# Kernel tuning notes

Hardware: AMD Instinct MI355X
Metric: run time of the kernel (lower is better)

## Reference

```python
import jax, jax.numpy as jnp
import numpy as np

N = 100000   # nodes
E = 600000   # edges (no self loops by construction)
F = 64       # feature_size
H = 2 * F    # hidden_size = 128
G = 32       # graphs in batch
L = N // G   # nodes per graph (equal-size graphs)
NEG_SLOPE = 0.2  # GATConv default leaky_relu slope


def setup_inputs() -> dict:
    key = jax.random.key(0)
    ks = jax.random.split(key, 16)
    x = jax.random.normal(ks[0], (N, F), jnp.float32)
    # edges guaranteed to have no self loops (PyG GAT removes then re-adds them)
    src = jax.random.randint(ks[1], (E,), 0, N)
    off = jax.random.randint(ks[2], (E,), 1, N)
    dst = (src + off) % N
    edge_index = jnp.stack([src, dst]).astype(jnp.int32)
    batch = (jnp.arange(N) // L).astype(jnp.int32)
    sF = 1.0 / np.sqrt(F)
    sH = 1.0 / np.sqrt(H)
    return {
        "x": x, "edge_index": edge_index, "batch": batch,
        "W0": jax.random.normal(ks[3], (F, H), jnp.float32) * sF,
        "b0": jnp.zeros((H,), jnp.float32),
        "Wg": jax.random.normal(ks[4], (H, H), jnp.float32) * sH,
        "att_src": jax.random.normal(ks[5], (H,), jnp.float32) * sH,
        "att_dst": jax.random.normal(ks[6], (H,), jnp.float32) * sH,
        "W1": jax.random.normal(ks[7], (H, H), jnp.float32) * sH,
        "b1": jnp.zeros((H,), jnp.float32),
        "W2": jax.random.normal(ks[8], (H, H), jnp.float32) * sH,
        "b2": jnp.zeros((H,), jnp.float32),
        "Wr": jax.random.normal(ks[9], (H, F), jnp.float32) * sH,
        "br": jnp.zeros((F,), jnp.float32),
    }


def _gcn(x, row, col, w, W, b):
    # PyG GCNConv (normalize=True); edges already include self loops, w holds edge weights.
    xw = x @ W
    deg = jax.ops.segment_sum(w, col, num_segments=N)
    dinv = jnp.where(deg > 0, deg, 1.0) ** -0.5
    dinv = jnp.where(deg > 0, dinv, 0.0)
    norm = dinv[row] * w * dinv[col]                      # [E+N]
    out = jax.ops.segment_sum(xw[row] * norm[:, None], col, num_segments=N)
    return out + b


def reference(x, edge_index, batch, W0, b0, Wg, att_src, att_dst, W1, b1, W2, b2, Wr, br):
    row, col = edge_index[0], edge_index[1]
    loops = jnp.arange(N, dtype=edge_index.dtype)
    row_f = jnp.concatenate([row, loops])                 # [E+N] with self loops
    col_f = jnp.concatenate([col, loops])

    # initial GCNConv (gcn_norm adds self loops with weight 1) + relu
    x = jax.nn.relu(_gcn(x, row_f, col_f, jnp.ones(E + N, x.dtype), W0, b0))

    # GATConv attention (heads=1); node output is discarded in the torch module
    xg = x @ Wg
    a_s = xg @ att_src
    a_d = xg @ att_dst
    e = jax.nn.leaky_relu(a_s[row_f] + a_d[col_f], NEG_SLOPE)
    m = jax.ops.segment_max(e, col_f, num_segments=N)
    ex = jnp.exp(e - m[col_f])
    alpha = ex / jax.ops.segment_sum(ex, col_f, num_segments=N)[col_f]

    # gcn_norm's add_remaining_self_loops replaces self-loop weights with 1.0
    w = alpha.at[E:].set(1.0)

    x = jax.nn.relu(_gcn(x, row_f, col_f, w, W1, b1))
    x = jax.nn.relu(_gcn(x, row_f, col_f, w, W2, b2))

    # readout: Dropout (eval -> identity) + Linear
    out = x @ Wr + br                                     # [N, F]

    # unbatch + pad_sequence (batch_first=True); batch ids are sorted
    counts = jax.ops.segment_sum(jnp.ones(N, jnp.int32), batch, num_segments=G)
    starts = jnp.concatenate([jnp.zeros(1, jnp.int32), jnp.cumsum(counts)[:-1].astype(jnp.int32)])
    pos = jnp.arange(N, dtype=jnp.int32) - starts[batch]
    emb = jnp.zeros((G, L, F), out.dtype).at[batch, pos].set(out)
    return emb
```

## Files before the change

kernel.cpp:

```cpp
#include <hip/hip_runtime.h>
#include <hip/hip_bf16.h>
#include <hip/hip_fp16.h>
#include <math.h>

#define NN 100000
#define EE 600000
#define FF 64
#define HH 128
#define CHUNK 1024
#define NCHUNK ((NN + CHUNK - 1) / CHUNK)
#define NCHUNKS_M (NN / 16)
#define PREP_ITEMS (NN * FF / 4 + 49280)

typedef unsigned short u16;
typedef unsigned int u32;
typedef __attribute__((ext_vector_type(8))) short bf16x8;
typedef __attribute__((ext_vector_type(4))) float f32x4;

__device__ __forceinline__ u16 f2bf(float f) {
    __hip_bfloat16 h = __float2bfloat16(f);
    return *(u16*)&h;
}
__device__ __forceinline__ float bf2f(u16 u) {
    unsigned int t = ((unsigned int)u) << 16;
    return *(float*)&t;
}
__device__ __forceinline__ u32 enc_meta(int r, float w) {
    u16 hb = __half_as_ushort(__float2half(w));
    return ((u32)r << 15) | (hb & 0x7fffu);
}
__device__ __forceinline__ void dec_meta(u32 u, int& r, float& w) {
    r = (int)(u >> 15);
    w = __half2float(__ushort_as_half((u16)(u & 0x7fffu)));
}


__global__ void build_k(const int* __restrict__ col, int* __restrict__ cnt,
                        const float* __restrict__ W0, const float* __restrict__ W1,
                        const float* __restrict__ W2, const float* __restrict__ Wr,
                        const float* __restrict__ Wg, const float* __restrict__ att_src,
                        const float* __restrict__ att_dst, const float* __restrict__ x,
                        u16* __restrict__ Wt0, u16* __restrict__ Wt1,
                        u16* __restrict__ Wt2, u16* __restrict__ Wtr,
                        float* __restrict__ vs, float* __restrict__ vd,
                        u16* __restrict__ xb) {
    int i = blockIdx.x * 256 + threadIdx.x;
    if (i < EE) {
        atomicAdd(&cnt[col[i]], 1);
        return;
    }
    i -= EE;
    if (i < NN * FF / 4) {
        float4 v = ((const float4*)x)[i];
        ushort4 o;
        o.x = f2bf(v.x); o.y = f2bf(v.y); o.z = f2bf(v.z); o.w = f2bf(v.w);
        ((ushort4*)xb)[i] = o;
        return;
    }
    i -= NN * FF / 4;
    if (i < 8192) {
        int n = i >> 6, k = i & 63;
        Wt0[i] = f2bf(W0[k * 128 + n]);
        return;
    }
    i -= 8192;
    if (i < 16384) {
        int n = i >> 7, k = i & 127;
        Wt1[i] = f2bf(W1[k * 128 + n]);
        return;
    }
    i -= 16384;
    if (i < 16384) {
        int n = i >> 7, k = i & 127;
        Wt2[i] = f2bf(W2[k * 128 + n]);
        return;
    }
    i -= 16384;
    if (i < 8192) {
        int n = i >> 7, k = i & 127;
        Wtr[i] = f2bf(Wr[k * 64 + n]);
        return;
    }
    i -= 8192;
    if (i < HH) {
        float s1 = 0.f, s2 = 0.f;
        for (int j = 0; j < HH; j++) {
            float w = Wg[i * HH + j];
            s1 += w * att_src[j];
            s2 += w * att_dst[j];
        }
        vs[i] = s1;
        vd[i] = s2;
    }
}

__global__ void chunksum_k(const int* __restrict__ cnt, int* __restrict__ chunk_sum,
                           float* __restrict__ dinv1) {
    int b = blockIdx.x, t = threadIdx.x;
    int base = b * CHUNK + t * 4;
    int s = 0;
    #pragma unroll
    for (int i = 0; i < 4; i++) {
        int idx = base + i;
        if (idx < NN) {
            int cv = cnt[idx];
            s += cv;
            dinv1[idx] = rsqrtf((float)cv + 1.0f);
        }
    }
    __shared__ int sm[4];
    for (int d = 32; d > 0; d >>= 1) s += __shfl_down(s, d);
    if ((t & 63) == 0) sm[t >> 6] = s;
    __syncthreads();
    if (t == 0) chunk_sum[b] = sm[0] + sm[1] + sm[2] + sm[3];
}

__global__ void colptr_k(const int* __restrict__ cnt, const int* __restrict__ chunk_sum,
                         int* __restrict__ col_ptr, int* __restrict__ cursor) {
    int b = blockIdx.x, t = threadIdx.x;
    __shared__ int base_off;
    if (t == 0) {
        int run = 0;
        for (int i = 0; i < b; i++) run += chunk_sum[i];
        base_off = run;
        if (b == 0) col_ptr[NN] = EE;
    }
    int base = b * CHUNK + t * 4;
    int c[4]; int tot = 0;
    #pragma unroll
    for (int i = 0; i < 4; i++) { int idx = base + i; c[i] = (idx < NN) ? cnt[idx] : 0; tot += c[i]; }
    __shared__ int s[256];
    s[t] = tot;
    __syncthreads();
    for (int d = 1; d < 256; d <<= 1) {
        int v = (t >= d) ? s[t - d] : 0;
        __syncthreads();
        s[t] += v;
        __syncthreads();
    }
    int excl = s[t] - tot;
    int off = base_off + excl;
    int pre = 0;
    #pragma unroll
    for (int i = 0; i < 4; i++) {
        int idx = base + i;
        if (idx < NN) {
            col_ptr[idx] = off + pre;
            cursor[idx] = off + pre;
        }
        pre += c[i];
    }
}

__global__ void fill_k(const int* __restrict__ row, const int* __restrict__ col,
                       int* __restrict__ cursor, const float* __restrict__ dinv1,
                       u32* __restrict__ meta1) {
    int e = blockIdx.x * 256 + threadIdx.x;
    if (e < EE) {
        int r = row[e], c = col[e];
        int slot = atomicAdd(&cursor[c], 1);
        meta1[slot] = enc_meta(r, dinv1[r] * dinv1[c]);
    }
}


__global__ __launch_bounds__(256, 8) void aggx_k(
    const u16* __restrict__ xb, const int* __restrict__ col_ptr, const u32* __restrict__ meta1,
    const float* __restrict__ dinv1, u16* __restrict__ xout) {
    int wid = threadIdx.x >> 6, lane = threadIdx.x & 63;
    int sub = lane >> 5;
    int c = blockIdx.x * 8 + wid * 2 + sub;
    int hl = lane & 31;
    int g = hl >> 3;
    int ch = (hl & 7) << 3;
    int beg = col_ptr[c], end = col_ptr[c + 1];
    float acc[8] = {};

    int pA = beg + g, pB = pA + 4;
    int rA = 0, rB = 0; float wA = 0.f, wB = 0.f;
    if (pA < end) dec_meta(meta1[pA], rA, wA);
    if (pB < end) dec_meta(meta1[pB], rB, wB);
    while (pA < end) {
        bool hb = pB < end;
        bf16x8 vA = *(const bf16x8*)&xb[(size_t)rA * FF + ch];
        bf16x8 vB;
        if (hb) vB = *(const bf16x8*)&xb[(size_t)rB * FF + ch];
        int pA2 = pA + 8, pB2 = pB + 8;
        int rA2 = 0, rB2 = 0; float wA2 = 0.f, wB2 = 0.f;
        if (pA2 < end) dec_meta(meta1[pA2], rA2, wA2);
        if (pB2 < end) dec_meta(meta1[pB2], rB2, wB2);
        #pragma unroll
        for (int j = 0; j < 8; j++) acc[j] = fmaf(bf2f((u16)vA[j]), wA, acc[j]);
        if (hb) {
            #pragma unroll
            for (int j = 0; j < 8; j++) acc[j] = fmaf(bf2f((u16)vB[j]), wB, acc[j]);
        }
        pA = pA2; pB = pB2; rA = rA2; rB = rB2; wA = wA2; wB = wB2;
    }
    #pragma unroll
    for (int j = 0; j < 8; j++) {
        acc[j] += __shfl_xor(acc[j], 8);
        acc[j] += __shfl_xor(acc[j], 16);
    }

    if (g == 0) {
        bf16x8 v = *(const bf16x8*)&xb[(size_t)c * FF + ch];
        float dc = dinv1[c];
        float ws = dc * dc;
        bf16x8 o;
        #pragma unroll
        for (int j = 0; j < 8; j++) {
            float t = fmaf(bf2f((u16)v[j]), ws, acc[j]);
            o[j] = (short)f2bf(t);
        }
        *(bf16x8*)&xout[(size_t)c * FF + ch] = o;
    }
}


__global__ __launch_bounds__(256) void gemm1_k(const u16* __restrict__ A,
                                               const u16* __restrict__ Wt0,
                                               const u16* __restrict__ Wt1,
                                               const float* __restrict__ bias,
                                               const float* __restrict__ vs, const float* __restrict__ vd,
                                               u16* __restrict__ Y, float* __restrict__ a_s,
                                               float* __restrict__ a_d) {
    constexpr int K = FF, N = HH, KK = K / 32, NT = N / 16, KK2 = HH / 32;
    constexpr int LSTRIDE = 136;
    __shared__ u16 lds[4][16 * LSTRIDE];
    int lane = threadIdx.x & 63, wid = threadIdx.x >> 6;
    int l15 = lane & 15, l4 = lane >> 4;
    int wg = blockIdx.x * 4 + wid;
    int nwaves = gridDim.x * 4;
    u16* myl = &lds[wid][0];

    bf16x8 a_frag[KK][NT];
    #pragma unroll
    for (int kk = 0; kk < KK; kk++)
        #pragma unroll
        for (int nt = 0; nt < NT; nt++)
            a_frag[kk][nt] = *(const bf16x8*)&Wt0[(size_t)(nt * 16 + l15) * K + kk * 32 + l4 * 8];

    for (int ch = wg; ch < NCHUNKS_M; ch += nwaves) {
        int row = ch * 16 + l15;
        bf16x8 b_frag[KK];
        #pragma unroll
        for (int kk = 0; kk < KK; kk++)
            b_frag[kk] = *(const bf16x8*)&A[(size_t)row * K + kk * 32 + l4 * 8];
        f32x4 acc[NT] = {};
        #pragma unroll
        for (int kk = 0; kk < KK; kk++)
            #pragma unroll
            for (int nt = 0; nt < NT; nt++)
                acc[nt] = __builtin_amdgcn_mfma_f32_16x16x32_bf16(a_frag[kk][nt], b_frag[kk],
                                                                  acc[nt], 0, 0, 0);
        float s1 = 0.f, s2 = 0.f;
        #pragma unroll
        for (int nt = 0; nt < NT; nt++) {
            f32x4 b4 = *(const f32x4*)&bias[nt * 16 + l4 * 4];
            f32x4 v4 = *(const f32x4*)&vs[nt * 16 + l4 * 4];
            f32x4 d4 = *(const f32x4*)&vd[nt * 16 + l4 * 4];
            float o0 = fmaxf(acc[nt][0] + b4[0], 0.f);
            float o1 = fmaxf(acc[nt][1] + b4[1], 0.f);
            float o2 = fmaxf(acc[nt][2] + b4[2], 0.f);
            float o3 = fmaxf(acc[nt][3] + b4[3], 0.f);
            ushort4 o;
            o.x = f2bf(o0); o.y = f2bf(o1); o.z = f2bf(o2); o.w = f2bf(o3);
            *(ushort4*)&myl[l15 * LSTRIDE + nt * 16 + l4 * 4] = o;
            s1 += o0 * v4[0] + o1 * v4[1] + o2 * v4[2] + o3 * v4[3];
            s2 += o0 * d4[0] + o1 * d4[1] + o2 * d4[2] + o3 * d4[3];
        }
        s1 += __shfl_xor(s1, 16); s1 += __shfl_xor(s1, 32);
        s2 += __shfl_xor(s2, 16); s2 += __shfl_xor(s2, 32);
        if (l4 == 0) {
            a_s[row] = s1;
            a_d[row] = s2;
        }
        bf16x8 b2[KK2];
        #pragma unroll
        for (int kk2 = 0; kk2 < KK2; kk2++)
            b2[kk2] = *(const bf16x8*)&myl[l15 * LSTRIDE + kk2 * 32 + l4 * 8];
        f32x4 acc2[NT] = {};
        #pragma unroll
        for (int kk2 = 0; kk2 < KK2; kk2++)
            #pragma unroll
            for (int nt = 0; nt < NT; nt++) {
                bf16x8 w1f = *(const bf16x8*)&Wt1[(size_t)(nt * 16 + l15) * HH + kk2 * 32 + l4 * 8];
                acc2[nt] = __builtin_amdgcn_mfma_f32_16x16x32_bf16(w1f, b2[kk2], acc2[nt], 0, 0, 0);
            }
        #pragma unroll
        for (int nt = 0; nt < NT; nt++) {
            ushort4 o;
            o.x = f2bf(acc2[nt][0]);
            o.y = f2bf(acc2[nt][1]);
            o.z = f2bf(acc2[nt][2]);
            o.w = f2bf(acc2[nt][3]);
            *(ushort4*)&Y[(size_t)row * HH + nt * 16 + l4 * 4] = o;
        }
    }
}


__global__ __launch_bounds__(256) void attn_k(const int* __restrict__ col_ptr,
                                              const u32* __restrict__ meta1,
                                              const float* __restrict__ a_s,
                                              const float* __restrict__ a_d,
                                              float* __restrict__ alpha,
                                              float* __restrict__ dinv2) {
    int lane = threadIdx.x & 63, wid = threadIdx.x >> 6;
    int grp = lane >> 3, idx = lane & 7;
    int c = blockIdx.x * 32 + wid * 8 + grp;
    if (c >= NN) return;
    int beg = col_ptr[c], end = col_ptr[c + 1];
    float ad = a_d[c];
    float es = a_s[c] + ad;
    es = (es > 0.f) ? es : 0.2f * es;
    float m = (idx == 0) ? es : -1e30f;
    float s = (idx == 0) ? 1.f : 0.f;
    for (int p = beg + idx; p < end; p += 8) {
        float e = a_s[meta1[p] >> 15] + ad;
        e = (e > 0.f) ? e : 0.2f * e;
        alpha[p] = e;
        float mn = fmaxf(m, e);
        s = s * expf(m - mn) + expf(e - mn);
        m = mn;
    }
    #pragma unroll
    for (int d = 1; d < 8; d <<= 1) {
        float mo = __shfl_xor(m, d);
        float so = __shfl_xor(s, d);
        float mn = fmaxf(m, mo);
        s = s * expf(m - mn) + so * expf(mo - mn);
        m = mn;
    }
    float inv = 1.f / s;
    float aself = expf(es - m) * inv;
    float d2 = rsqrtf(2.f - aself);
    if (idx == 0) dinv2[c] = d2;
    float sc = inv * d2;
    for (int p = beg + idx; p < end; p += 8)
        alpha[p] = expf(alpha[p] - m) * sc;
}

__global__ void w2_k(const u32* __restrict__ meta1, const float* __restrict__ dinv2,
                     const float* __restrict__ alpha, u32* __restrict__ meta2) {
    int p = blockIdx.x * 256 + threadIdx.x;
    if (p < EE) {
        u32 u = meta1[p];
        int r = (int)(u >> 15);
        float w = alpha[p] * dinv2[r];
        u16 hb = __half_as_ushort(__float2half(w));
        meta2[p] = (u & 0xffff8000u) | (hb & 0x7fffu);
    }
}


template <int NOUT, bool OUTF32>
__global__ __launch_bounds__(256, 8) void agg_gemm_k(
    const u16* __restrict__ xw, const int* __restrict__ col_ptr, const u32* __restrict__ meta,
    const float* __restrict__ dinv2, const float* __restrict__ bias_in,
    const u16* __restrict__ Wt, const float* __restrict__ bias_out, void* __restrict__ Y_) {
    constexpr int KK2 = HH / 32;
    constexpr int NT = NOUT / 16;
    constexpr int NT_W = NT / 4;
    constexpr int LSTRIDE = 136;
    __shared__ u16 lds[16 * LSTRIDE];
    int tid = threadIdx.x;
    int lane = tid & 63, wid = tid >> 6;
    int node = tid >> 4;
    int ch = (tid & 15) << 3;
    int cbase = blockIdx.x * 16;
    int c = cbase + node;
    int beg = col_ptr[c], end = col_ptr[c + 1];
    float acc[8] = {};

    int pA = beg, pB = beg + 1, pC = beg + 2, pD = beg + 3;
    int rA = 0, rB = 0, rC = 0, rD = 0;
    float wA = 0.f, wB = 0.f, wC = 0.f, wD = 0.f;
    if (pA < end) dec_meta(meta[pA], rA, wA);
    if (pB < end) dec_meta(meta[pB], rB, wB);
    if (pC < end) dec_meta(meta[pC], rC, wC);
    if (pD < end) dec_meta(meta[pD], rD, wD);
    while (pA < end) {
        bool hb = pB < end, hc = pC < end, hd = pD < end;
        bf16x8 vA = *(const bf16x8*)&xw[(size_t)rA * HH + ch];
        bf16x8 vB, vC, vD;
        if (hb) vB = *(const bf16x8*)&xw[(size_t)rB * HH + ch];
        if (hc) vC = *(const bf16x8*)&xw[(size_t)rC * HH + ch];
        if (hd) vD = *(const bf16x8*)&xw[(size_t)rD * HH + ch];
        pA += 4; pB += 4; pC += 4; pD += 4;
        int rA2 = 0, rB2 = 0, rC2 = 0, rD2 = 0;
        float wA2 = 0.f, wB2 = 0.f, wC2 = 0.f, wD2 = 0.f;
        if (pA < end) dec_meta(meta[pA], rA2, wA2);
        if (pB < end) dec_meta(meta[pB], rB2, wB2);
        if (pC < end) dec_meta(meta[pC], rC2, wC2);
        if (pD < end) dec_meta(meta[pD], rD2, wD2);
        #pragma unroll
        for (int j = 0; j < 8; j++) acc[j] = fmaf(bf2f((u16)vA[j]), wA, acc[j]);
        if (hb) {
            #pragma unroll
            for (int j = 0; j < 8; j++) acc[j] = fmaf(bf2f((u16)vB[j]), wB, acc[j]);
        }
        if (hc) {
            #pragma unroll
            for (int j = 0; j < 8; j++) acc[j] = fmaf(bf2f((u16)vC[j]), wC, acc[j]);
        }
        if (hd) {
            #pragma unroll
            for (int j = 0; j < 8; j++) acc[j] = fmaf(bf2f((u16)vD[j]), wD, acc[j]);
        }
        rA = rA2; rB = rB2; rC = rC2; rD = rD2;
        wA = wA2; wB = wB2; wC = wC2; wD = wD2;
    }
    {
        bf16x8 v = *(const bf16x8*)&xw[(size_t)c * HH + ch];
        float dc = dinv2[c];
        float ws = dc * dc;
        f32x4 b4a = *(const f32x4*)&bias_in[ch];
        f32x4 b4b = *(const f32x4*)&bias_in[ch + 4];
        bf16x8 o;
        #pragma unroll
        for (int j = 0; j < 8; j++) {
            float bj = (j < 4) ? b4a[j] : b4b[j - 4];
            float t = fmaxf(fmaf(bf2f((u16)v[j]), ws, acc[j]) + bj, 0.f);
            o[j] = (short)f2bf(t);
        }
        *(bf16x8*)&lds[node * LSTRIDE + ch] = o;
    }
    __syncthreads();

    int l15 = lane & 15, l4 = lane >> 4;
    bf16x8 b2[KK2];
    #pragma unroll
    for (int kk2 = 0; kk2 < KK2; kk2++)
        b2[kk2] = *(const bf16x8*)&lds[l15 * LSTRIDE + kk2 * 32 + l4 * 8];
    int row = cbase + l15;
    #pragma unroll
    for (int ntw = 0; ntw < NT_W; ntw++) {
        int nt = wid * NT_W + ntw;
        f32x4 acc2 = {};
        #pragma unroll
        for (int kk2 = 0; kk2 < KK2; kk2++) {
            bf16x8 wf = *(const bf16x8*)&Wt[(size_t)(nt * 16 + l15) * HH + kk2 * 32 + l4 * 8];
            acc2 = __builtin_amdgcn_mfma_f32_16x16x32_bf16(wf, b2[kk2], acc2, 0, 0, 0);
        }
        int col = nt * 16 + l4 * 4;
        if (OUTF32) {
            float4 o;
            f32x4 bo = *(const f32x4*)&bias_out[col];
            o.x = acc2[0] + bo[0];
            o.y = acc2[1] + bo[1];
            o.z = acc2[2] + bo[2];
            o.w = acc2[3] + bo[3];
            *(float4*)&((float*)Y_)[(size_t)row * NOUT + col] = o;
        } else {
            ushort4 o;
            o.x = f2bf(acc2[0]);
            o.y = f2bf(acc2[1]);
            o.z = f2bf(acc2[2]);
            o.w = f2bf(acc2[3]);
            *(ushort4*)&((u16*)Y_)[(size_t)row * NOUT + col] = o;
        }
    }
}


extern "C" void kernel_launch(void* const* d_in, const int* in_sizes, int n_in,
                              void* d_out, int out_size, void* d_ws, size_t ws_size,
                              hipStream_t stream) {
    const float* x = (const float*)d_in[0];
    const int* eidx = (const int*)d_in[1];
    const float* W0 = (const float*)d_in[3];
    const float* b0 = (const float*)d_in[4];
    const float* Wg = (const float*)d_in[5];
    const float* att_src = (const float*)d_in[6];
    const float* att_dst = (const float*)d_in[7];
    const float* W1 = (const float*)d_in[8];
    const float* b1 = (const float*)d_in[9];
    const float* W2 = (const float*)d_in[10];
    const float* b2 = (const float*)d_in[11];
    const float* Wr = (const float*)d_in[12];
    const float* br = (const float*)d_in[13];
    float* out = (float*)d_out;

    const int* erow = eidx;
    const int* ecol = eidx + EE;

    char* p = (char*)d_ws;
    auto alloc = [&](size_t bytes) {
        void* r = (void*)p;
        p += (bytes + 255) & ~(size_t)255;
        return r;
    };
    int* col_ptr = (int*)alloc((NN + 1) * sizeof(int));
    u32* meta1 = (u32*)alloc(EE * sizeof(u32));
    u32* meta2 = (u32*)alloc(EE * sizeof(u32));
    int* cnt = (int*)alloc(NN * sizeof(int));
    int* cursor = (int*)alloc(NN * sizeof(int));
    int* chunk_sum = (int*)alloc(128 * sizeof(int));
    float* alpha = (float*)alloc(EE * sizeof(float));
    float* dinv1 = (float*)alloc(NN * sizeof(float));
    float* dinv2 = (float*)alloc(NN * sizeof(float));
    float* a_s = (float*)alloc(NN * sizeof(float));
    float* a_d = (float*)alloc(NN * sizeof(float));
    float* vs = (float*)alloc(HH * sizeof(float));
    float* vd = (float*)alloc(HH * sizeof(float));
    u16* Wt0 = (u16*)alloc(8192 * sizeof(u16));
    u16* Wt1 = (u16*)alloc(16384 * sizeof(u16));
    u16* Wt2 = (u16*)alloc(16384 * sizeof(u16));
    u16* Wtr = (u16*)alloc(8192 * sizeof(u16));
    u16* xb = (u16*)alloc((size_t)NN * FF * sizeof(u16));
    u16* xaggb = (u16*)alloc((size_t)NN * FF * sizeof(u16));
    u16* bufA = (u16*)alloc((size_t)NN * HH * sizeof(u16));
    u16* bufB = (u16*)alloc((size_t)NN * HH * sizeof(u16));

    hipMemsetAsync(cnt, 0, NN * sizeof(int), stream);

    build_k<<<(EE + PREP_ITEMS + 255) / 256, 256, 0, stream>>>(
        ecol, cnt, W0, W1, W2, Wr, Wg, att_src, att_dst, x,
        Wt0, Wt1, Wt2, Wtr, vs, vd, xb);
    chunksum_k<<<NCHUNK, 256, 0, stream>>>(cnt, chunk_sum, dinv1);
    colptr_k<<<NCHUNK, 256, 0, stream>>>(cnt, chunk_sum, col_ptr, cursor);
    fill_k<<<(EE + 255) / 256, 256, 0, stream>>>(erow, ecol, cursor, dinv1, meta1);

    int aggGrid = NN / 8;
    const int GG = 512;

    aggx_k<<<aggGrid, 256, 0, stream>>>(xb, col_ptr, meta1, dinv1, xaggb);
    gemm1_k<<<GG, 256, 0, stream>>>(xaggb, Wt0, Wt1, b0, vs, vd, bufB, a_s, a_d);
    attn_k<<<(NN + 31) / 32, 256, 0, stream>>>(col_ptr, meta1, a_s, a_d, alpha, dinv2);
    w2_k<<<(EE + 255) / 256, 256, 0, stream>>>(meta1, dinv2, alpha, meta2);
    agg_gemm_k<HH, false><<<NCHUNKS_M, 256, 0, stream>>>(bufB, col_ptr, meta2, dinv2, b1,
                                                         Wt2, nullptr, bufA);
    agg_gemm_k<FF, true><<<NCHUNKS_M, 256, 0, stream>>>(bufA, col_ptr, meta2, dinv2, b2,
                                                        Wtr, br, out);
}
```

Before: 236.0 us.

## Group nodes by in-degree for load-balanced aggregation-GEMM blocks

Builds a degree-sorted node permutation with a histogram, a scan and a scatter, and makes both agg_gemm kernels process nodes in that order. Each block of 16 nodes then has similar in-degree, which is meant to cut divergence and waiting on the slowest node within a wave. The cost is three extra small kernels and a memset. Output rows become scattered writes, and the gathered col_ptr accesses lose locality.

```diff
diff --git a/kernel.cpp b/kernel.cpp
--- a/kernel.cpp
+++ b/kernel.cpp
@@ -11,6 +11,7 @@
 #define NCHUNK ((NN + CHUNK - 1) / CHUNK)
 #define NCHUNKS_M (NN / 16)
 #define PREP_ITEMS (NN * FF / 4 + 49280)
+#define NBIN 64
 
 typedef unsigned short u16;
 typedef unsigned int u32;
@@ -161,6 +162,46 @@
         int slot = atomicAdd(&cursor[c], 1);
         meta1[slot] = enc_meta(r, dinv1[r] * dinv1[c]);
     }
+}
+
+
+__global__ void deghist_k(const int* __restrict__ cnt, int* __restrict__ bins) {
+    __shared__ int h[NBIN];
+    int t = threadIdx.x;
+    if (t < NBIN) h[t] = 0;
+    __syncthreads();
+    int i = blockIdx.x * 256 + t;
+    if (i < NN) {
+        int d = min(cnt[i], NBIN - 1);
+        atomicAdd(&h[d], 1);
+    }
+    __syncthreads();
+    if (t < NBIN && h[t] > 0) atomicAdd(&bins[t], h[t]);
+}
+
+__global__ void degscan_k(const int* __restrict__ bins, int* __restrict__ bincur) {
+    if (threadIdx.x == 0) {
+        int run = 0;
+        for (int d = 0; d < NBIN; d++) { bincur[d] = run; run += bins[d]; }
+    }
+}
+
+__global__ void permfill_k(const int* __restrict__ cnt, int* __restrict__ bincur,
+                           int* __restrict__ perm) {
+    __shared__ int h[NBIN], base[NBIN];
+    int t = threadIdx.x;
+    if (t < NBIN) h[t] = 0;
+    __syncthreads();
+    int i = blockIdx.x * 256 + t;
+    int d = 0, myoff = 0;
+    if (i < NN) {
+        d = min(cnt[i], NBIN - 1);
+        myoff = atomicAdd(&h[d], 1);
+    }
+    __syncthreads();
+    if (t < NBIN && h[t] > 0) base[t] = atomicAdd(&bincur[t], h[t]);
+    __syncthreads();
+    if (i < NN) perm[base[d] + myoff] = i;
 }
 
 
@@ -358,8 +399,9 @@
 template <int NOUT, bool OUTF32>
 __global__ __launch_bounds__(256, 8) void agg_gemm_k(
     const u16* __restrict__ xw, const int* __restrict__ col_ptr, const u32* __restrict__ meta,
-    const float* __restrict__ dinv2, const float* __restrict__ bias_in,
-    const u16* __restrict__ Wt, const float* __restrict__ bias_out, void* __restrict__ Y_) {
+    const int* __restrict__ perm, const float* __restrict__ dinv2,
+    const float* __restrict__ bias_in, const u16* __restrict__ Wt,
+    const float* __restrict__ bias_out, void* __restrict__ Y_) {
     constexpr int KK2 = HH / 32;
     constexpr int NT = NOUT / 16;
     constexpr int NT_W = NT / 4;
@@ -370,7 +412,7 @@
     int node = tid >> 4;
     int ch = (tid & 15) << 3;
     int cbase = blockIdx.x * 16;
-    int c = cbase + node;
+    int c = perm[cbase + node];
     int beg = col_ptr[c], end = col_ptr[c + 1];
     float acc[8] = {};
 
@@ -434,7 +476,7 @@
     #pragma unroll
     for (int kk2 = 0; kk2 < KK2; kk2++)
         b2[kk2] = *(const bf16x8*)&lds[l15 * LSTRIDE + kk2 * 32 + l4 * 8];
-    int row = cbase + l15;
+    int row = perm[cbase + l15];
     #pragma unroll
     for (int ntw = 0; ntw < NT_W; ntw++) {
         int nt = wid * NT_W + ntw;
@@ -498,6 +540,9 @@
     int* cnt = (int*)alloc(NN * sizeof(int));
     int* cursor = (int*)alloc(NN * sizeof(int));
     int* chunk_sum = (int*)alloc(128 * sizeof(int));
+    int* bins = (int*)alloc(NBIN * sizeof(int));
+    int* bincur = (int*)alloc(NBIN * sizeof(int));
+    int* perm = (int*)alloc(NN * sizeof(int));
     float* alpha = (float*)alloc(EE * sizeof(float));
     float* dinv1 = (float*)alloc(NN * sizeof(float));
     float* dinv2 = (float*)alloc(NN * sizeof(float));
@@ -515,6 +560,7 @@
     u16* bufB = (u16*)alloc((size_t)NN * HH * sizeof(u16));
 
     hipMemsetAsync(cnt, 0, NN * sizeof(int), stream);
+    hipMemsetAsync(bins, 0, NBIN * sizeof(int), stream);
 
     build_k<<<(EE + PREP_ITEMS + 255) / 256, 256, 0, stream>>>(
         ecol, cnt, W0, W1, W2, Wr, Wg, att_src, att_dst, x,
@@ -522,6 +568,9 @@
     chunksum_k<<<NCHUNK, 256, 0, stream>>>(cnt, chunk_sum, dinv1);
     colptr_k<<<NCHUNK, 256, 0, stream>>>(cnt, chunk_sum, col_ptr, cursor);
     fill_k<<<(EE + 255) / 256, 256, 0, stream>>>(erow, ecol, cursor, dinv1, meta1);
+    deghist_k<<<(NN + 255) / 256, 256, 0, stream>>>(cnt, bins);
+    degscan_k<<<1, 64, 0, stream>>>(bins, bincur);
+    permfill_k<<<(NN + 255) / 256, 256, 0, stream>>>(cnt, bincur, perm);
 
     int aggGrid = NN / 8;
     const int GG = 512;
@@ -530,8 +579,8 @@
     gemm1_k<<<GG, 256, 0, stream>>>(xaggb, Wt0, Wt1, b0, vs, vd, bufB, a_s, a_d);
     attn_k<<<(NN + 31) / 32, 256, 0, stream>>>(col_ptr, meta1, a_s, a_d, alpha, dinv2);
     w2_k<<<(EE + 255) / 256, 256, 0, stream>>>(meta1, dinv2, alpha, meta2);
-    agg_gemm_k<HH, false><<<NCHUNKS_M, 256, 0, stream>>>(bufB, col_ptr, meta2, dinv2, b1,
-                                                         Wt2, nullptr, bufA);
-    agg_gemm_k<FF, true><<<NCHUNKS_M, 256, 0, stream>>>(bufA, col_ptr, meta2, dinv2, b2,
-                                                        Wtr, br, out);
-}
+    agg_gemm_k<HH, false><<<NCHUNKS_M, 256, 0, stream>>>(bufB, col_ptr, meta2, perm, dinv2,
+                                                         b1, Wt2, nullptr, bufA);
+    agg_gemm_k<FF, true><<<NCHUNKS_M, 256, 0, stream>>>(bufA, col_ptr, meta2, perm, dinv2,
+                                                        b2, Wtr, br, out);
+}
```

Measured after the change: 247.4 us. 4.8% more time.
